# Kernel optimization log

Hardware: AMD Instinct MI355X
Metric: run time of the kernel (lower is better)

The kernel has to match this reference:

```python
import jax, jax.numpy as jnp
import numpy as np

N_VAR = 1_000_000
N_CON = 500_000
N_EDGE = 8_000_000
H = 10  # n_h_feats


def setup_inputs() -> dict:
    key = jax.random.key(0)
    ks = jax.random.split(key, 20)
    f32 = jnp.float32
    s = 0.3  # weight init scale
    return {
        'var_c': jax.random.normal(ks[0], (N_VAR,), f32),
        'var_x': jax.random.normal(ks[1], (N_VAR,), f32),
        'con_b': jax.random.normal(ks[2], (N_CON,), f32),
        'edge_src': jax.random.randint(ks[3], (N_EDGE,), 0, N_VAR, jnp.int32),
        'edge_dst': jax.random.randint(ks[4], (N_EDGE,), 0, N_CON, jnp.int32),
        'edge_w': jax.random.uniform(ks[5], (N_EDGE,), f32),
        'Wv': jax.random.normal(ks[6], (2, H), f32) * s,
        'bv': jnp.zeros((H,), f32),
        'Wc': jax.random.normal(ks[7], (1, H), f32) * s,
        'bc': jnp.zeros((H,), f32),
        'W1': jax.random.normal(ks[8], (H, H), f32) * s,
        'b1': jnp.zeros((H,), f32),
        'W2': jax.random.normal(ks[9], (H, H), f32) * s,
        'b2': jnp.zeros((H,), f32),
        'Wo1': jax.random.normal(ks[10], (H, H), f32) * s,
        'bo1': jnp.zeros((H,), f32),
        'Wo2': jax.random.normal(ks[11], (H, H), f32) * s,
        'bo2': jnp.zeros((H,), f32),
        'Wo3': jax.random.normal(ks[12], (H, 1), f32) * s,
        'bo3': jnp.zeros((1,), f32),
    }


def _graph_conv(feat_src, src, dst, w, n_dst, deg_src, deg_dst, W, b):
    # DGL GraphConv, norm='both', with edge weights:
    # h = D_src^{-1/2} x ; m_e = h[src_e] * w_e ; agg = scatter_sum(m, dst)
    # out = (D_dst^{-1/2} agg) @ W + b
    h = feat_src * jax.lax.rsqrt(deg_src)[:, None]
    m = h[src] * w[:, None]                      # [E, H] gather + scale
    agg = jax.ops.segment_sum(m, dst, num_segments=n_dst)  # scatter-add
    agg = agg * jax.lax.rsqrt(deg_dst)[:, None]
    return agg @ W + b


def reference(var_c, var_x, con_b, edge_src, edge_dst, edge_w,
              Wv, bv, Wc, bc, W1, b1, W2, b2, Wo1, bo1, Wo2, bo2, Wo3, bo3):
    # node embeddings
    var_feat = jnp.stack([var_c, var_x], axis=1)            # [N_VAR, 2]
    con_feat = con_b.reshape(-1, 1)                          # [N_CON, 1]
    X_var = jax.nn.relu(var_feat @ Wv + bv)                  # [N_VAR, H]
    X_con = jax.nn.relu(con_feat @ Wc + bc)                  # computed in original; unused by GraphConv (no dst-feat term)

    ones_e = jnp.ones((edge_src.shape[0],), jnp.float32)
    deg_var = jnp.maximum(jax.ops.segment_sum(ones_e, edge_src, num_segments=N_VAR), 1.0)
    deg_con = jnp.maximum(jax.ops.segment_sum(ones_e, edge_dst, num_segments=N_CON), 1.0)

    # conv1['con'] is overwritten by conv2['con'] in the original (v2c src feats are X_var both times)
    h_con = jax.nn.relu(_graph_conv(X_var, edge_src, edge_dst, edge_w, N_CON, deg_var, deg_con, W2, b2))
    # likewise conv1['var'] is overwritten by conv2['var'] (c2v src feats are h_con both times)
    h_var = jax.nn.relu(_graph_conv(h_con, edge_dst, edge_src, edge_w, N_VAR, deg_con, deg_var, W2, b2))

    z = jax.nn.relu(h_var @ Wo1 + bo1)
    z = jax.nn.relu(z @ Wo2 + bo2)
    logit = z @ Wo3 + bo3                                    # [N_VAR, 1]
    # dgl.readout_nodes(op='mean') over a single batched graph
    return jnp.mean(logit, axis=0, keepdims=True)            # [1, 1]
```

## Files before the change

kernel.cpp:

```cpp
#include <hip/hip_runtime.h>

#define NVAR 1000000
#define NCON 500000
#define EPB 4096
#define FCAP 4480


__global__ __launch_bounds__(256) void kA_hist2(const int4* __restrict__ src4,
                                                const int4* __restrict__ dst4,
                                                unsigned* __restrict__ bhV,
                                                unsigned* __restrict__ bhC,
                                                int ne4, int nblk) {
    __shared__ unsigned hv[1024], hc[1024];
    int tid = threadIdx.x, b = blockIdx.x;
    for (int t = tid; t < 1024; t += 256) { hv[t] = 0; hc[t] = 0; }
    __syncthreads();
    int beg = b * (EPB / 4), end = min(ne4, beg + (EPB / 4));
    for (int i = beg + tid; i < end; i += 256) {
        int4 s = src4[i];
        int4 d = dst4[i];
        atomicAdd(&hv[s.x >> 10], 1u); atomicAdd(&hv[s.y >> 10], 1u);
        atomicAdd(&hv[s.z >> 10], 1u); atomicAdd(&hv[s.w >> 10], 1u);
        atomicAdd(&hc[d.x >> 9], 1u);  atomicAdd(&hc[d.y >> 9], 1u);
        atomicAdd(&hc[d.z >> 9], 1u);  atomicAdd(&hc[d.w >> 9], 1u);
    }
    __syncthreads();
    for (int t = tid; t < 1024; t += 256) {
        bhV[(size_t)t * nblk + b] = hv[t];
        bhC[(size_t)t * nblk + b] = hc[t];
    }
}

__global__ __launch_bounds__(256) void kA_scat(const int* __restrict__ keys,
                                               const int* __restrict__ vals,
                                               const float* __restrict__ w,
                                               const unsigned int* __restrict__ scanned,
                                               int2* __restrict__ bucketed,
                                               int ne, int shift, int nblk) {
    __shared__ unsigned int h[1024];
    __shared__ unsigned int lb[1024];
    __shared__ unsigned int gb[1024];
    __shared__ unsigned int sc[256];
    __shared__ int2 stage[EPB];
    int tid = threadIdx.x, b = blockIdx.x;
    for (int t = tid; t < 1024; t += 256) {
        h[t] = 0;
        gb[t] = scanned[(size_t)t * nblk + b];
    }
    __syncthreads();
    int beg = b * EPB, end = min(ne, beg + EPB), cnt = end - beg;
    int cnt4 = cnt >> 2;
    const int4* keys4 = (const int4*)(keys + beg);
    for (int i = tid; i < cnt4; i += 256) {
        int4 k = keys4[i];
        atomicAdd(&h[k.x >> shift], 1u);
        atomicAdd(&h[k.y >> shift], 1u);
        atomicAdd(&h[k.z >> shift], 1u);
        atomicAdd(&h[k.w >> shift], 1u);
    }
    for (int i = cnt4 * 4 + tid; i < cnt; i += 256) atomicAdd(&h[keys[beg + i] >> shift], 1u);
    __syncthreads();
    unsigned v0, v1, v2, v3;
    int q = tid * 4;
    v0 = h[q]; v1 = h[q + 1]; v2 = h[q + 2]; v3 = h[q + 3];
    sc[tid] = v0 + v1 + v2 + v3;
    __syncthreads();
    for (int dd = 1; dd < 256; dd <<= 1) {
        unsigned add = (tid >= dd) ? sc[tid - dd] : 0u;
        __syncthreads();
        sc[tid] += add;
        __syncthreads();
    }
    unsigned ex = (tid == 0) ? 0u : sc[tid - 1];
    lb[q]     = ex;
    lb[q + 1] = ex + v0;
    lb[q + 2] = ex + v0 + v1;
    lb[q + 3] = ex + v0 + v1 + v2;
    __syncthreads();
    for (int t = tid; t < 1024; t += 256) h[t] = 0;
    __syncthreads();
    unsigned mask = (1u << shift) - 1u;
    const int4* vals4 = (const int4*)(vals + beg);
    const float4* w4 = (const float4*)(w + beg);
    for (int i = tid; i < cnt4; i += 256) {
        int4 k = keys4[i];
        int4 v = vals4[i];
        float4 ww = w4[i];
        {
            unsigned bkt = (unsigned)k.x >> shift;
            unsigned r = atomicAdd(&h[bkt], 1u);
            stage[lb[bkt] + r] = make_int2(__float_as_int(ww.x),
                                           (v.x << shift) | (unsigned)(k.x & (int)mask));
        }
        {
            unsigned bkt = (unsigned)k.y >> shift;
            unsigned r = atomicAdd(&h[bkt], 1u);
            stage[lb[bkt] + r] = make_int2(__float_as_int(ww.y),
                                           (v.y << shift) | (unsigned)(k.y & (int)mask));
        }
        {
            unsigned bkt = (unsigned)k.z >> shift;
            unsigned r = atomicAdd(&h[bkt], 1u);
            stage[lb[bkt] + r] = make_int2(__float_as_int(ww.z),
                                           (v.z << shift) | (unsigned)(k.z & (int)mask));
        }
        {
            unsigned bkt = (unsigned)k.w >> shift;
            unsigned r = atomicAdd(&h[bkt], 1u);
            stage[lb[bkt] + r] = make_int2(__float_as_int(ww.w),
                                           (v.w << shift) | (unsigned)(k.w & (int)mask));
        }
    }
    for (int i = cnt4 * 4 + tid; i < cnt; i += 256) {
        int k = keys[beg + i];
        unsigned bkt = (unsigned)k >> shift;
        unsigned r = atomicAdd(&h[bkt], 1u);
        stage[lb[bkt] + r] = make_int2(__float_as_int(w[beg + i]),
                                       (vals[beg + i] << shift) | (unsigned)(k & (int)mask));
    }
    __syncthreads();
    for (int i = tid; i < cnt; i += 256) {
        unsigned bb = 0;
#pragma unroll
        for (int step = 512; step > 0; step >>= 1) {
            unsigned cand = bb + step;
            if (cand < 1024 && lb[cand] <= (unsigned)i) bb = cand;
        }
        bucketed[gb[bb] + ((unsigned)i - lb[bb])] = stage[i];
    }
}

__global__ __launch_bounds__(256) void kDeg(const int2* __restrict__ bucketed,
                                            const unsigned* __restrict__ scanned,
                                            unsigned* __restrict__ deg,
                                            int nnodes, int nblk, int lowbits) {
    __shared__ unsigned h[1024];
    int d = blockIdx.x, tid = threadIdx.x;
    int W = 1 << lowbits;
    unsigned mask = (unsigned)(W - 1);
    unsigned base = scanned[(size_t)d * nblk], next = scanned[(size_t)(d + 1) * nblk];
    for (int t = tid; t < W; t += 256) h[t] = 0;
    __syncthreads();
    for (unsigned i = base + tid; i < next; i += 256)
        atomicAdd(&h[(unsigned)bucketed[i].y & mask], 1u);
    __syncthreads();
    int lo = d << lowbits;
    for (int t = tid; t < W; t += 256) {
        int node = lo + t;
        if (node < nnodes) deg[node] = h[t];
    }
}

__global__ __launch_bounds__(256) void k_scan_blocks(const unsigned int* in,
                                                     unsigned int* out,
                                                     unsigned int* bsum,
                                                     int n) {
    __shared__ unsigned int sT[256];
    int base = blockIdx.x * 1024 + threadIdx.x * 4;
    unsigned int v0 = 0, v1 = 0, v2 = 0, v3 = 0;
    if (base + 3 < n) {
        uint4 u = *(const uint4*)(in + base);
        v0 = u.x; v1 = u.y; v2 = u.z; v3 = u.w;
    } else {
        if (base     < n) v0 = in[base];
        if (base + 1 < n) v1 = in[base + 1];
        if (base + 2 < n) v2 = in[base + 2];
        if (base + 3 < n) v3 = in[base + 3];
    }
    sT[threadIdx.x] = v0 + v1 + v2 + v3;
    __syncthreads();
    for (int d = 1; d < 256; d <<= 1) {
        unsigned int add = (threadIdx.x >= (unsigned)d) ? sT[threadIdx.x - d] : 0u;
        __syncthreads();
        sT[threadIdx.x] += add;
        __syncthreads();
    }
    unsigned int excl = (threadIdx.x == 0) ? 0u : sT[threadIdx.x - 1];
    if (base     < n) out[base]     = excl;
    if (base + 1 < n) out[base + 1] = excl + v0;
    if (base + 2 < n) out[base + 2] = excl + v0 + v1;
    if (base + 3 < n) out[base + 3] = excl + v0 + v1 + v2;
    if (threadIdx.x == 255 && bsum) bsum[blockIdx.x] = sT[255];
}

__global__ __launch_bounds__(256) void k_scan_mid(const unsigned* __restrict__ in,
                                                  unsigned* __restrict__ out, int n) {
    __shared__ unsigned sT[256];
    __shared__ unsigned carry;
    if (threadIdx.x == 0) carry = 0;
    __syncthreads();
    for (int base = 0; base < n; base += 256) {
        int i = base + threadIdx.x;
        unsigned v = (i < n) ? in[i] : 0u;
        sT[threadIdx.x] = v;
        __syncthreads();
        for (int d = 1; d < 256; d <<= 1) {
            unsigned add = (threadIdx.x >= (unsigned)d) ? sT[threadIdx.x - d] : 0u;
            __syncthreads();
            sT[threadIdx.x] += add;
            __syncthreads();
        }
        unsigned excl = carry + ((threadIdx.x == 0) ? 0u : sT[threadIdx.x - 1]);
        if (i < n) out[i] = excl;
        __syncthreads();
        if (threadIdx.x == 255) carry += sT[255];
        __syncthreads();
    }
}

__global__ __launch_bounds__(256) void k_scan_add(unsigned int* __restrict__ data,
                                                  const unsigned int* __restrict__ bscan,
                                                  int n) {
    int base = blockIdx.x * 1024 + threadIdx.x * 4;
    unsigned int add = bscan[blockIdx.x];
    if (base + 3 < n) {
        uint4 u = *(const uint4*)(data + base);
        u.x += add; u.y += add; u.z += add; u.w += add;
        *(uint4*)(data + base) = u;
    } else {
        if (base     < n) data[base]     += add;
        if (base + 1 < n) data[base + 1] += add;
        if (base + 2 < n) data[base + 2] += add;
        if (base + 3 < n) data[base + 3] += add;
    }
}


__global__ __launch_bounds__(256) void k_pack(const float* __restrict__ var_c,
                                              const float* __restrict__ var_x,
                                              const unsigned int* __restrict__ deg_var,
                                              float4* __restrict__ vcr, int n) {
    int i = blockIdx.x * blockDim.x + threadIdx.x;
    if (i >= n) return;
    float rs = rsqrtf(fmaxf((float)deg_var[i], 1.0f));
    vcr[i] = make_float4(var_c[i], var_x[i], rs, 0.0f);
}

#define EMBADD(e)                                                             \
    {                                                                         \
        float4 vv = vcr[(size_t)(e).y];                                       \
        float we = __int_as_float((e).x);                                     \
        float t0 = fmaf(vv.x, wv0[0], fmaf(vv.y, wv1[0], bvr[0]));            \
        float t1 = fmaf(vv.x, wv0[1], fmaf(vv.y, wv1[1], bvr[1]));            \
        float t2 = fmaf(vv.x, wv0[2], fmaf(vv.y, wv1[2], bvr[2]));            \
        float t3 = fmaf(vv.x, wv0[3], fmaf(vv.y, wv1[3], bvr[3]));            \
        acc.x = fmaf(we, fmaxf(t0, 0.f) * vv.z, acc.x);                       \
        acc.y = fmaf(we, fmaxf(t1, 0.f) * vv.z, acc.y);                       \
        acc.z = fmaf(we, fmaxf(t2, 0.f) * vv.z, acc.z);                       \
        acc.w = fmaf(we, fmaxf(t3, 0.f) * vv.z, acc.w);                       \
    }

#define EMB4(eA, eB, eC, eD)                                                  \
    {                                                                         \
        float4 vA = vcr[(size_t)(eA).y];                                      \
        float4 vB = vcr[(size_t)(eB).y];                                      \
        float4 vC = vcr[(size_t)(eC).y];                                      \
        float4 vD = vcr[(size_t)(eD).y];                                      \
        float wA = __int_as_float((eA).x), wB = __int_as_float((eB).x);       \
        float wC = __int_as_float((eC).x), wD = __int_as_float((eD).x);       \
        float t0, t1, t2, t3;                                                 \
        t0 = fmaf(vA.x, wv0[0], fmaf(vA.y, wv1[0], bvr[0]));                  \
        t1 = fmaf(vA.x, wv0[1], fmaf(vA.y, wv1[1], bvr[1]));                  \
        t2 = fmaf(vA.x, wv0[2], fmaf(vA.y, wv1[2], bvr[2]));                  \
        t3 = fmaf(vA.x, wv0[3], fmaf(vA.y, wv1[3], bvr[3]));                  \
        acc.x = fmaf(wA, fmaxf(t0, 0.f) * vA.z, acc.x);                       \
        acc.y = fmaf(wA, fmaxf(t1, 0.f) * vA.z, acc.y);                       \
        acc.z = fmaf(wA, fmaxf(t2, 0.f) * vA.z, acc.z);                       \
        acc.w = fmaf(wA, fmaxf(t3, 0.f) * vA.z, acc.w);                       \
        t0 = fmaf(vB.x, wv0[0], fmaf(vB.y, wv1[0], bvr[0]));                  \
        t1 = fmaf(vB.x, wv0[1], fmaf(vB.y, wv1[1], bvr[1]));                  \
        t2 = fmaf(vB.x, wv0[2], fmaf(vB.y, wv1[2], bvr[2]));                  \
        t3 = fmaf(vB.x, wv0[3], fmaf(vB.y, wv1[3], bvr[3]));                  \
        acc.x = fmaf(wB, fmaxf(t0, 0.f) * vB.z, acc.x);                       \
        acc.y = fmaf(wB, fmaxf(t1, 0.f) * vB.z, acc.y);                       \
        acc.z = fmaf(wB, fmaxf(t2, 0.f) * vB.z, acc.z);                       \
        acc.w = fmaf(wB, fmaxf(t3, 0.f) * vB.z, acc.w);                       \
        t0 = fmaf(vC.x, wv0[0], fmaf(vC.y, wv1[0], bvr[0]));                  \
        t1 = fmaf(vC.x, wv0[1], fmaf(vC.y, wv1[1], bvr[1]));                  \
        t2 = fmaf(vC.x, wv0[2], fmaf(vC.y, wv1[2], bvr[2]));                  \
        t3 = fmaf(vC.x, wv0[3], fmaf(vC.y, wv1[3], bvr[3]));                  \
        acc.x = fmaf(wC, fmaxf(t0, 0.f) * vC.z, acc.x);                       \
        acc.y = fmaf(wC, fmaxf(t1, 0.f) * vC.z, acc.y);                       \
        acc.z = fmaf(wC, fmaxf(t2, 0.f) * vC.z, acc.z);                       \
        acc.w = fmaf(wC, fmaxf(t3, 0.f) * vC.z, acc.w);                       \
        t0 = fmaf(vD.x, wv0[0], fmaf(vD.y, wv1[0], bvr[0]));                  \
        t1 = fmaf(vD.x, wv0[1], fmaf(vD.y, wv1[1], bvr[1]));                  \
        t2 = fmaf(vD.x, wv0[2], fmaf(vD.y, wv1[2], bvr[2]));                  \
        t3 = fmaf(vD.x, wv0[3], fmaf(vD.y, wv1[3], bvr[3]));                  \
        acc.x = fmaf(wD, fmaxf(t0, 0.f) * vD.z, acc.x);                       \
        acc.y = fmaf(wD, fmaxf(t1, 0.f) * vD.z, acc.y);                       \
        acc.z = fmaf(wD, fmaxf(t2, 0.f) * vD.z, acc.z);                       \
        acc.w = fmaf(wD, fmaxf(t3, 0.f) * vD.z, acc.w);                       \
    }

__global__ __launch_bounds__(512) void kF_con(const int2* __restrict__ bucketed,
                                              const unsigned* __restrict__ scanned,
                                              const unsigned* __restrict__ startC,
                                              const float4* __restrict__ vcr,
                                              const float* __restrict__ Wv,
                                              const float* __restrict__ bv,
                                              const float* __restrict__ W2,
                                              const float* __restrict__ b2,
                                              float* __restrict__ hs, int nblk, int netot) {
    __shared__ unsigned sraw[257], cr[256];
    __shared__ float sWv[20], sbv[10], sW[100], sb[10];
    __shared__ int2 stage[FCAP];
    int tid = threadIdx.x;
    int d = blockIdx.x >> 1, half = blockIdx.x & 1;
    int gbase = (d << 9) + half * 256;
    for (int t = tid; t < 100; t += 512) sW[t] = W2[t];
    if (tid < 10) sb[tid] = b2[tid];
    if (tid < 20) sWv[tid] = Wv[tid];
    if (tid >= 20 && tid < 30) sbv[tid - 20] = bv[tid - 20];
    for (int t = tid; t < 257; t += 512) {
        int g = gbase + t;
        sraw[t] = (g < NCON) ? startC[g] : (unsigned)netot;
    }
    if (tid < 256) cr[tid] = 0;
    __syncthreads();
    unsigned own_beg = sraw[0], own_end = sraw[256];
    bool fit = (int)(own_end - own_beg) <= FCAP;
    unsigned bbase = scanned[(size_t)d * nblk];
    unsigned bnext = scanned[(size_t)(d + 1) * nblk];
    int bsz = (int)(bnext - bbase);
    if (fit) {
        for (int i = tid; i < bsz; i += 512) {
            int2 p = bucketed[bbase + i];
            unsigned low = (unsigned)p.y & 511u;
            if ((int)(low >> 8) == half) {
                unsigned nl = low & 255u;
                unsigned r = atomicAdd(&cr[nl], 1u);
                stage[sraw[nl] - own_beg + r] = make_int2(p.x, p.y >> 9);
            }
        }
    }
    __syncthreads();
    int quad = tid >> 2, lane = tid & 3, c0 = lane * 4;
    float wv0[4], wv1[4], bvr[4];
#pragma unroll
    for (int k = 0; k < 4; k++) {
        int j = c0 + k;
        wv0[k] = (j < 10) ? sWv[j] : 0.f;
        wv1[k] = (j < 10) ? sWv[10 + j] : 0.f;
        bvr[k] = (j < 10) ? sbv[j] : 0.f;
    }
#pragma unroll
    for (int rr = 0; rr < 2; rr++) {
        int nl = rr * 128 + quad;
        int g = gbase + nl;
        if (g >= NCON) continue;
        float4 acc = make_float4(0.f, 0.f, 0.f, 0.f);
        unsigned cnt;
        if (fit) {
            unsigned beg = sraw[nl] - own_beg;
            cnt = cr[nl];
            unsigned end = beg + cnt, p = beg;
            for (; p + 4 <= end; p += 4) {
                int2 e0 = stage[p], e1 = stage[p + 1], e2 = stage[p + 2], e3 = stage[p + 3];
                EMB4(e0, e1, e2, e3);
            }
            for (; p < end; ++p) {
                int2 e = stage[p];
                EMBADD(e);
            }
        } else {
            cnt = 0;
            unsigned target = (unsigned)(half * 256 + nl);
            for (int i = 0; i < bsz; ++i) {
                int2 p = bucketed[bbase + i];
                if (((unsigned)p.y & 511u) == target) {
                    ++cnt;
                    int2 e = make_int2(p.x, p.y >> 9);
                    EMBADD(e);
                }
            }
        }
        float rs = rsqrtf(fmaxf((float)cnt, 1.0f));
        float a[10];
        a[0] = __shfl(acc.x, 0, 4); a[1] = __shfl(acc.y, 0, 4);
        a[2] = __shfl(acc.z, 0, 4); a[3] = __shfl(acc.w, 0, 4);
        a[4] = __shfl(acc.x, 1, 4); a[5] = __shfl(acc.y, 1, 4);
        a[6] = __shfl(acc.z, 1, 4); a[7] = __shfl(acc.w, 1, 4);
        a[8] = __shfl(acc.x, 2, 4); a[9] = __shfl(acc.y, 2, 4);
#pragma unroll
        for (int j = 0; j < 10; j++) a[j] *= rs;
        float o[12];
#pragma unroll
        for (int k = 0; k < 10; k++) {
            float t = sb[k];
#pragma unroll
            for (int j = 0; j < 10; j++) t = fmaf(a[j], sW[j * 10 + k], t);
            o[k] = fmaxf(t, 0.0f) * rs;
        }
        o[10] = 0.0f; o[11] = 0.0f;
        float4 wv = (lane < 3) ? make_float4(o[c0], o[c0 + 1], o[c0 + 2], o[c0 + 3])
                               : make_float4(0.f, 0.f, 0.f, 0.f);
        *(float4*)(hs + (size_t)g * 16 + c0) = wv;
    }
}

#define GATHER4(eA, eB, eC, eD, TAB)                                          \
    {                                                                         \
        float4 v0 = *(const float4*)(TAB + (size_t)(eA).y * 16 + c0);         \
        float4 v1 = *(const float4*)(TAB + (size_t)(eB).y * 16 + c0);         \
        float4 v2 = *(const float4*)(TAB + (size_t)(eC).y * 16 + c0);         \
        float4 v3 = *(const float4*)(TAB + (size_t)(eD).y * 16 + c0);         \
        float w0 = __int_as_float((eA).x), w1 = __int_as_float((eB).x);       \
        float w2 = __int_as_float((eC).x), w3 = __int_as_float((eD).x);       \
        acc.x = fmaf(w0, v0.x, acc.x); acc.y = fmaf(w0, v0.y, acc.y);         \
        acc.z = fmaf(w0, v0.z, acc.z); acc.w = fmaf(w0, v0.w, acc.w);         \
        acc.x = fmaf(w1, v1.x, acc.x); acc.y = fmaf(w1, v1.y, acc.y);         \
        acc.z = fmaf(w1, v1.z, acc.z); acc.w = fmaf(w1, v1.w, acc.w);         \
        acc.x = fmaf(w2, v2.x, acc.x); acc.y = fmaf(w2, v2.y, acc.y);         \
        acc.z = fmaf(w2, v2.z, acc.z); acc.w = fmaf(w2, v2.w, acc.w);         \
        acc.x = fmaf(w3, v3.x, acc.x); acc.y = fmaf(w3, v3.y, acc.y);         \
        acc.z = fmaf(w3, v3.z, acc.z); acc.w = fmaf(w3, v3.w, acc.w);         \
    }

__global__ __launch_bounds__(512) void kF_fin(const int2* __restrict__ bucketed,
                                              const unsigned* __restrict__ scanned,
                                              const unsigned* __restrict__ startV,
                                              const float* __restrict__ feat,
                                              const float* __restrict__ W2,
                                              const float* __restrict__ b2,
                                              const float* __restrict__ Wo1,
                                              const float* __restrict__ bo1,
                                              const float* __restrict__ Wo2,
                                              const float* __restrict__ bo2,
                                              const float* __restrict__ Wo3,
                                              const float* __restrict__ bo3,
                                              double* __restrict__ partials, int nblk, int netot) {
    __shared__ unsigned sraw[513], cr[512];
    __shared__ float sW2[100], sb2[10], sWo1[100], sbo1[10], sWo2[100], sbo2[10], sWo3[10], sbo3v;
    __shared__ int2 stage[FCAP];
    __shared__ double red[512];
    int tid = threadIdx.x;
    int d = blockIdx.x >> 1, half = blockIdx.x & 1;
    int gbase = (d << 10) + half * 512;
    for (int t = tid; t < 100; t += 512) { sW2[t] = W2[t]; sWo1[t] = Wo1[t]; sWo2[t] = Wo2[t]; }
    if (tid < 10) {
        sb2[tid] = b2[tid]; sbo1[tid] = bo1[tid]; sbo2[tid] = bo2[tid]; sWo3[tid] = Wo3[tid];
    }
    if (tid == 0) sbo3v = bo3[0];
    for (int t = tid; t < 513; t += 512) {
        int g = gbase + t;
        sraw[t] = (g < NVAR) ? startV[g] : (unsigned)netot;
    }
    cr[tid] = 0;
    __syncthreads();
    unsigned own_beg = sraw[0], own_end = sraw[512];
    bool fit = (int)(own_end - own_beg) <= FCAP;
    unsigned bbase = scanned[(size_t)d * nblk];
    unsigned bnext = scanned[(size_t)(d + 1) * nblk];
    int bsz = (int)(bnext - bbase);
    if (fit) {
        for (int i = tid; i < bsz; i += 512) {
            int2 p = bucketed[bbase + i];
            unsigned low = (unsigned)p.y & 1023u;
            if ((int)(low >> 9) == half) {
                unsigned nl = low & 511u;
                unsigned r = atomicAdd(&cr[nl], 1u);
                stage[sraw[nl] - own_beg + r] = make_int2(p.x, p.y >> 10);
            }
        }
    }
    __syncthreads();
    int quad = tid >> 2, lane = tid & 3, c0 = lane * 4;
    double accd = 0.0;
#pragma unroll
    for (int rr = 0; rr < 4; rr++) {
        int nl = rr * 128 + quad;
        int g = gbase + nl;
        if (g >= NVAR) continue;
        float4 acc = make_float4(0.f, 0.f, 0.f, 0.f);
        unsigned cnt;
        if (fit) {
            unsigned beg = sraw[nl] - own_beg;
            cnt = cr[nl];
            unsigned end = beg + cnt, p = beg;
            for (; p + 4 <= end; p += 4) {
                int2 e0 = stage[p], e1 = stage[p + 1], e2 = stage[p + 2], e3 = stage[p + 3];
                GATHER4(e0, e1, e2, e3, feat);
            }
            for (; p < end; ++p) {
                int2 e = stage[p];
                float4 v = *(const float4*)(feat + (size_t)e.y * 16 + c0);
                float we = __int_as_float(e.x);
                acc.x = fmaf(we, v.x, acc.x); acc.y = fmaf(we, v.y, acc.y);
                acc.z = fmaf(we, v.z, acc.z); acc.w = fmaf(we, v.w, acc.w);
            }
        } else {
            cnt = 0;
            unsigned target = (unsigned)(half * 512 + nl);
            for (int i = 0; i < bsz; ++i) {
                int2 p = bucketed[bbase + i];
                if (((unsigned)p.y & 1023u) == target) {
                    ++cnt;
                    float4 v = *(const float4*)(feat + (size_t)((unsigned)p.y >> 10) * 16 + c0);
                    float we = __int_as_float(p.x);
                    acc.x = fmaf(we, v.x, acc.x); acc.y = fmaf(we, v.y, acc.y);
                    acc.z = fmaf(we, v.z, acc.z); acc.w = fmaf(we, v.w, acc.w);
                }
            }
        }
        float rs = rsqrtf(fmaxf((float)cnt, 1.0f));
        float a[10];
        a[0] = __shfl(acc.x, 0, 4); a[1] = __shfl(acc.y, 0, 4);
        a[2] = __shfl(acc.z, 0, 4); a[3] = __shfl(acc.w, 0, 4);
        a[4] = __shfl(acc.x, 1, 4); a[5] = __shfl(acc.y, 1, 4);
        a[6] = __shfl(acc.z, 1, 4); a[7] = __shfl(acc.w, 1, 4);
        a[8] = __shfl(acc.x, 2, 4); a[9] = __shfl(acc.y, 2, 4);
#pragma unroll
        for (int j = 0; j < 10; j++) a[j] *= rs;
        float hh[10], z[10];
#pragma unroll
        for (int k = 0; k < 10; k++) {
            float t = sb2[k];
#pragma unroll
            for (int j = 0; j < 10; j++) t = fmaf(a[j], sW2[j * 10 + k], t);
            hh[k] = fmaxf(t, 0.0f);
        }
#pragma unroll
        for (int k = 0; k < 10; k++) {
            float t = sbo1[k];
#pragma unroll
            for (int j = 0; j < 10; j++) t = fmaf(hh[j], sWo1[j * 10 + k], t);
            z[k] = fmaxf(t, 0.0f);
        }
        float t3 = sbo3v;
#pragma unroll
        for (int k = 0; k < 10; k++) {
            float t = sbo2[k];
#pragma unroll
            for (int j = 0; j < 10; j++) t = fmaf(z[j], sWo2[j * 10 + k], t);
            t = fmaxf(t, 0.0f);
            t3 = fmaf(t, sWo3[k], t3);
        }
        if (lane == 0) accd += (double)t3;
    }
    red[tid] = accd;
    __syncthreads();
    for (int off = 256; off > 0; off >>= 1) {
        if (tid < off) red[tid] += red[tid + off];
        __syncthreads();
    }
    if (tid == 0) partials[blockIdx.x] = red[0];
}

__global__ __launch_bounds__(256) void k_out(const double* __restrict__ partials, int np,
                                             float* __restrict__ out) {
    __shared__ double red[256];
    double a = 0.0;
    for (int i = threadIdx.x; i < np; i += blockDim.x) a += partials[i];
    red[threadIdx.x] = a;
    __syncthreads();
    for (int off = 128; off > 0; off >>= 1) {
        if (threadIdx.x < off) red[threadIdx.x] += red[threadIdx.x + off];
        __syncthreads();
    }
    if (threadIdx.x == 0) out[0] = (float)(red[0] / (double)NVAR);
}


extern "C" void kernel_launch(void* const* d_in, const int* in_sizes, int n_in,
                              void* d_out, int out_size, void* d_ws, size_t ws_size,
                              hipStream_t stream) {
    const float* var_c  = (const float*)d_in[0];
    const float* var_x  = (const float*)d_in[1];
    const int*   e_src  = (const int*)d_in[3];
    const int*   e_dst  = (const int*)d_in[4];
    const float* e_w    = (const float*)d_in[5];
    const float* Wv     = (const float*)d_in[6];
    const float* bv     = (const float*)d_in[7];
    const float* W2     = (const float*)d_in[12];
    const float* b2     = (const float*)d_in[13];
    const float* Wo1    = (const float*)d_in[14];
    const float* bo1    = (const float*)d_in[15];
    const float* Wo2    = (const float*)d_in[16];
    const float* bo2    = (const float*)d_in[17];
    const float* Wo3    = (const float*)d_in[18];
    const float* bo3    = (const float*)d_in[19];
    float* out = (float*)d_out;
    const int ne = in_sizes[3];
    (void)n_in; (void)out_size; (void)ws_size;

    const int B = 256;
    const int nblkA = (ne + EPB - 1) / EPB;
    const int scanN = 1024 * nblkA;
    const int NBs   = (scanN + 1023) / 1024;
    const int BKV   = (NVAR + 1023) >> 10;
    const int BKC   = (NCON + 511) >> 9;
    const int NBV   = (NVAR + 1023) / 1024;
    const int NBC   = (NCON + 1023) / 1024;
    const int ne4   = ne / 4;

    char* ws = (char*)d_ws;
    size_t off = 0;
    auto walloc = [&](size_t bytes) {
        void* p = ws + off;
        off = (off + bytes + 255) & ~(size_t)255;
        return p;
    };

    int2*     bucketedV = (int2*)walloc((size_t)ne * 8);
    int2*     bucketedC = (int2*)walloc((size_t)ne * 8);
    float4*   vcr       = (float4*)walloc((size_t)NVAR * 16);
    float*    hs64      = (float*)walloc((size_t)NCON * 16 * 4);
    unsigned* scannedV  = (unsigned*)walloc((size_t)scanN * 4);
    unsigned* scannedC  = (unsigned*)walloc((size_t)scanN * 4);
    unsigned* bhV       = (unsigned*)walloc((size_t)scanN * 4);
    unsigned* bhC       = (unsigned*)walloc((size_t)scanN * 4);
    unsigned* bsumA     = (unsigned*)walloc(8192);
    unsigned* bscanA    = (unsigned*)walloc(8192);
    double*   partials  = (double*)walloc((size_t)(BKV * 2) * 8 + 64);
    unsigned* deg_var   = bhV;
    unsigned* deg_con   = bhC;

    kA_hist2<<<nblkA, B, 0, stream>>>((const int4*)e_src, (const int4*)e_dst,
                                      bhV, bhC, ne4, nblkA);

    k_scan_blocks<<<NBs, B, 0, stream>>>(bhV, scannedV, bsumA, scanN);
    k_scan_mid   <<<1,   B, 0, stream>>>(bsumA, bscanA, NBs);
    k_scan_add   <<<NBs, B, 0, stream>>>(scannedV, bscanA, scanN);
    k_scan_blocks<<<NBs, B, 0, stream>>>(bhC, scannedC, bsumA, scanN);
    k_scan_mid   <<<1,   B, 0, stream>>>(bsumA, bscanA, NBs);
    k_scan_add   <<<NBs, B, 0, stream>>>(scannedC, bscanA, scanN);

    kA_scat<<<nblkA, B, 0, stream>>>(e_src, e_dst, e_w, scannedV, bucketedV, ne, 10, nblkA);

    kDeg<<<BKV, B, 0, stream>>>(bucketedV, scannedV, deg_var, NVAR, nblkA, 10);

    k_pack<<<(NVAR + B - 1) / B, B, 0, stream>>>(var_c, var_x, deg_var, vcr, NVAR);

    k_scan_blocks<<<NBV, B, 0, stream>>>(deg_var, deg_var, bsumA, NVAR);
    k_scan_mid   <<<1,   B, 0, stream>>>(bsumA, bscanA, NBV);
    k_scan_add   <<<NBV, B, 0, stream>>>(deg_var, bscanA, NVAR);

    kA_scat<<<nblkA, B, 0, stream>>>(e_dst, e_src, e_w, scannedC, bucketedC, ne, 9, nblkA);

    kDeg<<<BKC, B, 0, stream>>>(bucketedC, scannedC, deg_con, NCON, nblkA, 9);
    k_scan_blocks<<<NBC, B, 0, stream>>>(deg_con, deg_con, bsumA, NCON);
    k_scan_mid   <<<1,   B, 0, stream>>>(bsumA, bscanA, NBC);
    k_scan_add   <<<NBC, B, 0, stream>>>(deg_con, bscanA, NCON);

    kF_con<<<BKC * 2, 512, 0, stream>>>(bucketedC, scannedC, deg_con, vcr, Wv, bv,
                                        W2, b2, hs64, nblkA, ne);

    kF_fin<<<BKV * 2, 512, 0, stream>>>(bucketedV, scannedV, deg_var, hs64, W2, b2,
                                        Wo1, bo1, Wo2, bo2, Wo3, bo3, partials, nblkA, ne);

    k_out<<<1, B, 0, stream>>>(partials, BKV * 2, out);
}
```

Before: 614.1 us.

## Double edges per scatter block, record bucket ids, fuse degree and pack

Doubles the number of edges each bucketing block handles, which halves the block count and the size of the per-block histogram and scan arrays. Each staged entry now records its bucket id in shared memory, so the write-out loop no longer does a binary search over bucket offsets. The var-degree count and the feature packing step are merged into one kernel, removing a launch and a reread of the degree array. The larger shared staging buffer (about 80 KB per block) may reduce occupancy, and fewer blocks means less parallelism in the histogram and scatter passes.

Result: faster. 564.3 us (-8.1%).

```diff
diff --git a/kernel.cpp b/kernel.cpp
--- a/kernel.cpp
+++ b/kernel.cpp
@@ -2,7 +2,7 @@
 
 #define NVAR 1000000
 #define NCON 500000
-#define EPB 4096
+#define EPB 8192
 #define FCAP 4480
 
 
@@ -42,6 +42,7 @@
     __shared__ unsigned int gb[1024];
     __shared__ unsigned int sc[256];
     __shared__ int2 stage[EPB];
+    __shared__ unsigned short sbkt[EPB];
     int tid = threadIdx.x, b = blockIdx.x;
     for (int t = tid; t < 1024; t += 256) {
         h[t] = 0;
@@ -89,43 +90,48 @@
         {
             unsigned bkt = (unsigned)k.x >> shift;
             unsigned r = atomicAdd(&h[bkt], 1u);
-            stage[lb[bkt] + r] = make_int2(__float_as_int(ww.x),
-                                           (v.x << shift) | (unsigned)(k.x & (int)mask));
+            unsigned slot = lb[bkt] + r;
+            stage[slot] = make_int2(__float_as_int(ww.x),
+                                    (v.x << shift) | (unsigned)(k.x & (int)mask));
+            sbkt[slot] = (unsigned short)bkt;
         }
         {
             unsigned bkt = (unsigned)k.y >> shift;
             unsigned r = atomicAdd(&h[bkt], 1u);
-            stage[lb[bkt] + r] = make_int2(__float_as_int(ww.y),
-                                           (v.y << shift) | (unsigned)(k.y & (int)mask));
+            unsigned slot = lb[bkt] + r;
+            stage[slot] = make_int2(__float_as_int(ww.y),
+                                    (v.y << shift) | (unsigned)(k.y & (int)mask));
+            sbkt[slot] = (unsigned short)bkt;
         }
         {
             unsigned bkt = (unsigned)k.z >> shift;
             unsigned r = atomicAdd(&h[bkt], 1u);
-            stage[lb[bkt] + r] = make_int2(__float_as_int(ww.z),
-                                           (v.z << shift) | (unsigned)(k.z & (int)mask));
+            unsigned slot = lb[bkt] + r;
+            stage[slot] = make_int2(__float_as_int(ww.z),
+                                    (v.z << shift) | (unsigned)(k.z & (int)mask));
+            sbkt[slot] = (unsigned short)bkt;
         }
         {
             unsigned bkt = (unsigned)k.w >> shift;
             unsigned r = atomicAdd(&h[bkt], 1u);
-            stage[lb[bkt] + r] = make_int2(__float_as_int(ww.w),
-                                           (v.w << shift) | (unsigned)(k.w & (int)mask));
+            unsigned slot = lb[bkt] + r;
+            stage[slot] = make_int2(__float_as_int(ww.w),
+                                    (v.w << shift) | (unsigned)(k.w & (int)mask));
+            sbkt[slot] = (unsigned short)bkt;
         }
     }
     for (int i = cnt4 * 4 + tid; i < cnt; i += 256) {
         int k = keys[beg + i];
         unsigned bkt = (unsigned)k >> shift;
         unsigned r = atomicAdd(&h[bkt], 1u);
-        stage[lb[bkt] + r] = make_int2(__float_as_int(w[beg + i]),
-                                       (vals[beg + i] << shift) | (unsigned)(k & (int)mask));
+        unsigned slot = lb[bkt] + r;
+        stage[slot] = make_int2(__float_as_int(w[beg + i]),
+                                (vals[beg + i] << shift) | (unsigned)(k & (int)mask));
+        sbkt[slot] = (unsigned short)bkt;
     }
     __syncthreads();
     for (int i = tid; i < cnt; i += 256) {
-        unsigned bb = 0;
-#pragma unroll
-        for (int step = 512; step > 0; step >>= 1) {
-            unsigned cand = bb + step;
-            if (cand < 1024 && lb[cand] <= (unsigned)i) bb = cand;
-        }
+        unsigned bb = sbkt[i];
         bucketed[gb[bb] + ((unsigned)i - lb[bb])] = stage[i];
     }
 }
@@ -148,6 +154,33 @@
     for (int t = tid; t < W; t += 256) {
         int node = lo + t;
         if (node < nnodes) deg[node] = h[t];
+    }
+}
+
+__global__ __launch_bounds__(256) void kDegPackV(const int2* __restrict__ bucketed,
+                                                 const unsigned* __restrict__ scanned,
+                                                 const float* __restrict__ var_c,
+                                                 const float* __restrict__ var_x,
+                                                 unsigned* __restrict__ deg,
+                                                 float4* __restrict__ vcr,
+                                                 int nnodes, int nblk) {
+    __shared__ unsigned h[1024];
+    int d = blockIdx.x, tid = threadIdx.x;
+    unsigned base = scanned[(size_t)d * nblk], next = scanned[(size_t)(d + 1) * nblk];
+    for (int t = tid; t < 1024; t += 256) h[t] = 0;
+    __syncthreads();
+    for (unsigned i = base + tid; i < next; i += 256)
+        atomicAdd(&h[(unsigned)bucketed[i].y & 1023u], 1u);
+    __syncthreads();
+    int lo = d << 10;
+    for (int t = tid; t < 1024; t += 256) {
+        int node = lo + t;
+        if (node < nnodes) {
+            unsigned dg = h[t];
+            deg[node] = dg;
+            float rs = rsqrtf(fmaxf((float)dg, 1.0f));
+            vcr[node] = make_float4(var_c[node], var_x[node], rs, 0.0f);
+        }
     }
 }
 
@@ -225,16 +258,6 @@
     }
 }
 
-
-__global__ __launch_bounds__(256) void k_pack(const float* __restrict__ var_c,
-                                              const float* __restrict__ var_x,
-                                              const unsigned int* __restrict__ deg_var,
-                                              float4* __restrict__ vcr, int n) {
-    int i = blockIdx.x * blockDim.x + threadIdx.x;
-    if (i >= n) return;
-    float rs = rsqrtf(fmaxf((float)deg_var[i], 1.0f));
-    vcr[i] = make_float4(var_c[i], var_x[i], rs, 0.0f);
-}
 
 #define EMBADD(e)                                                             \
     {                                                                         \
@@ -628,9 +651,8 @@
 
     kA_scat<<<nblkA, B, 0, stream>>>(e_src, e_dst, e_w, scannedV, bucketedV, ne, 10, nblkA);
 
-    kDeg<<<BKV, B, 0, stream>>>(bucketedV, scannedV, deg_var, NVAR, nblkA, 10);
-
-    k_pack<<<(NVAR + B - 1) / B, B, 0, stream>>>(var_c, var_x, deg_var, vcr, NVAR);
+    kDegPackV<<<BKV, B, 0, stream>>>(bucketedV, scannedV, var_c, var_x,
+                                     deg_var, vcr, NVAR, nblkA);
 
     k_scan_blocks<<<NBV, B, 0, stream>>>(deg_var, deg_var, bsumA, NVAR);
     k_scan_mid   <<<1,   B, 0, stream>>>(bsumA, bscanA, NBV);
```
